# Performance work log

Measured on AMD Instinct MI355X. Metric: run time of the kernel, lower is better.

The kernel has to match this reference:

```python
import jax, jax.numpy as jnp
import numpy as np

B, IDF, CDF, H, Wd, L = 16, 128, 256, 128, 128, 64


def setup_inputs() -> dict:
    key = jax.random.key(0)
    k1, k2, k3, k4 = jax.random.split(key, 4)
    x = jax.random.normal(k1, (B, IDF, H, Wd), dtype=jnp.float32)
    context = jax.random.normal(k2, (B, CDF, L), dtype=jnp.float32)
    W = jax.random.normal(k3, (IDF, CDF), dtype=jnp.float32) * 0.02
    mask = jax.random.bernoulli(k4, 0.3, (B, L))
    # guarantee at least one unmasked word per row so the softmax is finite
    mask = mask.at[:, 0].set(False)
    return {"x": x, "context": context, "W": W, "mask": mask}


def reference(x, context, W, mask):
    # x: [B, idf, H, W]  context: [B, cdf, L]  W: [idf, cdf]  mask: [B, L] bool
    b, c, h, w = x.shape
    P = h * w
    l = context.shape[2]
    target = x.reshape(b, c, P)                       # [B, idf, P]
    # Conv1x1 over context (cdf -> idf)
    source = jnp.einsum('oc,bcl->bol', W, context)    # [B, idf, L]
    # QK^T: [B, P, idf] x [B, idf, L] -> [B, P, L]
    attn = jnp.einsum('bip,bil->bpl', target, source)
    attn = attn.reshape(b * P, l)
    # faithful to torch: mask.repeat(P, 1) tiled over the flattened rows
    m = jnp.tile(mask, (P, 1))                        # [B*P, L]
    attn = jnp.where(m, -jnp.inf, attn)
    attn = jax.nn.softmax(attn, axis=1).reshape(b, P, l)
    attnT = jnp.swapaxes(attn, 1, 2)                  # [B, L, P]
    # weighted context: [B, idf, L] x [B, L, P] -> [B, idf, P]
    weight = jnp.einsum('bil,blp->bip', source, attnT).reshape(b, c, h, w)
    attn_out = attnT.reshape(b, l, h, w)
    return weight, attn_out
```

## Files before the change

### kernel.cpp

```cpp
#include <hip/hip_runtime.h>
#include <hip/hip_bf16.h>
#include <hip/hip_fp16.h>

#define NB  16
#define IDF 128
#define CDF 256
#define LL  64
#define PP  16384
#define PXB 256
#define XPITCH 260

typedef _Float16 f16;
typedef _Float16 f16x4 __attribute__((ext_vector_type(4)));
typedef _Float16 f16x8 __attribute__((ext_vector_type(8)));
typedef float    f32x4 __attribute__((ext_vector_type(4)));

#define BAR() do { asm volatile("s_waitcnt lgkmcnt(0)" ::: "memory"); \
                   __builtin_amdgcn_s_barrier(); } while (0)

__global__ void src_pack_kernel(const float* __restrict__ Wm,
                                const float* __restrict__ ctx,
                                f16* __restrict__ srcF,
                                f16* __restrict__ srcT,
                                const unsigned char* __restrict__ mask_raw,
                                unsigned long long* __restrict__ mbits) {
    if (blockIdx.x == 0) {
        __shared__ int is_u8;
        const int tid = threadIdx.x;
        if (tid == 0) is_u8 = 0;
        if (tid < 16) mbits[tid] = 0ULL;
        __syncthreads();
        unsigned char byt[4];
        #pragma unroll
        for (int q = 0; q < 4; ++q) {
            int k = tid + q * 256;
            byt[q] = mask_raw[k];
            if ((k & 3) != 0 && byt[q] != 0) atomicOr(&is_u8, 1);
        }
        __syncthreads();
        #pragma unroll
        for (int q = 0; q < 4; ++q) {
            int k = tid + q * 256;
            int masked;
            if (is_u8) masked = (byt[q] != 0);
            else       masked = (((const int*)mask_raw)[k] != 0);
            if (masked) atomicOr(&mbits[k >> 6], 1ULL << (unsigned)(k & 63));
        }
    }

    int g = blockIdx.x * 256 + threadIdx.x;
    int l = g & (LL - 1);
    int i = (g >> 6) & (IDF - 1);
    int b = g >> 13;
    const float* wrow = Wm + (size_t)i * CDF;
    const float* ccol = ctx + (size_t)b * CDF * LL + l;
    float s = 0.f;
    #pragma unroll 8
    for (int c = 0; c < CDF; ++c)
        s = fmaf(wrow[c], ccol[(size_t)c * LL], s);
    f16 h = (f16)s;
    srcF[g] = h;
    srcT[((size_t)b * LL + l) * IDF + i] = h;
}

__global__ __launch_bounds__(256, 2)
void attn_mfma_kernel(const float* __restrict__ x,
                      const f16* __restrict__ srcT,
                      const f16* __restrict__ srcF,
                      const unsigned long long* __restrict__ mbits,
                      float* __restrict__ weight,
                      float* __restrict__ attn_out) {
    __shared__ __align__(16) unsigned char s_srcT[LL * 256];
    __shared__ __align__(16) unsigned char s_srcF[IDF * 128];
    __shared__ __align__(16) unsigned char s_u[34816];

    float* s_xpA = (float*)s_u;
    float* s_xpB = (float*)(s_u + 16640);

    const int b    = blockIdx.y;
    const int tid  = threadIdx.x;
    const int wv   = tid >> 6;
    const int lane = tid & 63;
    const int c    = lane & 15;
    const int g    = lane >> 4;
    const int cs   = (c & 7) << 4;

    f16* s_pw = (f16*)s_u + (size_t)wv * (64 * 68);

    const int bxs = (blockIdx.x & 7) * 4 + (blockIdx.x >> 3);
    const int pwb = bxs * (2 * PXB);
    const float* xb0 = x + (size_t)b * IDF * PP + pwb + wv * 64 + c;
    const float* xb1 = xb0 + PXB;

    unsigned mlo[4], mhi[4];
    #pragma unroll
    for (int r = 0; r < 4; ++r) {
        unsigned long long m = mbits[4 * g + r];
        mlo[r] = (unsigned)m;
        mhi[r] = (unsigned)(m >> 32);
    }

    float xfa[32], xfb[32];
    f16x8 xh0[4], xh1[4];
    f32x4 acc[4][4];
    f16x8 pa[4][2];

#define QK_LOAD(BUF, KS, XB)                                                \
    {   _Pragma("unroll")                                                   \
        for (int pt = 0; pt < 4; ++pt)                                      \
            _Pragma("unroll")                                               \
            for (int j = 0; j < 8; ++j)                                     \
                BUF[pt * 8 + j] =                                           \
                    (XB)[(size_t)((KS) * 32 + 8 * g + j) * PP + pt * 16];   \
    }

#define QK_CONV(BUF, XH)                                                    \
    {   _Pragma("unroll")                                                   \
        for (int pt = 0; pt < 4; ++pt)                                      \
            _Pragma("unroll")                                               \
            for (int j = 0; j < 8; ++j) XH[pt][j] = (f16)BUF[pt * 8 + j];   \
    }

#define QK_STEP_H(XH, KS)                                                   \
    {   _Pragma("unroll")                                                   \
        for (int nt = 0; nt < 4; ++nt) {                                    \
            const f16x8 bt = *reinterpret_cast<const f16x8*>(               \
                s_srcT + (nt * 16 + c) * 256 + (((KS) * 64 + 16 * g) ^ cs));\
            _Pragma("unroll")                                               \
            for (int pt = 0; pt < 4; ++pt)                                  \
                acc[pt][nt] = __builtin_amdgcn_mfma_f32_16x16x32_f16(       \
                    XH[pt], bt, acc[pt][nt], 0, 0, 0);                      \
        } }

#define QK_STEP(BUF, KS)                                                    \
    {   f16x8 xa_[4];                                                       \
        QK_CONV(BUF, xa_)                                                   \
        QK_STEP_H(xa_, KS) }

#define ACC_ZERO()                                                          \
    {   _Pragma("unroll")                                                   \
        for (int pt = 0; pt < 4; ++pt)                                      \
            _Pragma("unroll")                                               \
            for (int nt = 0; nt < 4; ++nt)                                  \
                acc[pt][nt] = (f32x4){0.f, 0.f, 0.f, 0.f}; }

#define SOFTMAX()                                                           \
    {   _Pragma("unroll")                                                   \
        for (int r = 0; r < 4; ++r) {                                       \
            const unsigned m0 = (mlo[r] >> c) & 1u;                         \
            const unsigned m1 = (mlo[r] >> (16 + c)) & 1u;                  \
            const unsigned m2 = (mhi[r] >> c) & 1u;                         \
            const unsigned m3 = (mhi[r] >> (16 + c)) & 1u;                  \
            _Pragma("unroll")                                               \
            for (int pt = 0; pt < 4; ++pt) {                                \
                if (m0) acc[pt][0][r] = -INFINITY;                          \
                if (m1) acc[pt][1][r] = -INFINITY;                          \
                if (m2) acc[pt][2][r] = -INFINITY;                          \
                if (m3) acc[pt][3][r] = -INFINITY;                          \
            }                                                               \
        }                                                                   \
        _Pragma("unroll")                                                   \
        for (int pt = 0; pt < 4; ++pt) {                                    \
            _Pragma("unroll")                                               \
            for (int r = 0; r < 4; ++r) {                                   \
                float mx = fmaxf(fmaxf(acc[pt][0][r], acc[pt][1][r]),       \
                                 fmaxf(acc[pt][2][r], acc[pt][3][r]));      \
                mx = fmaxf(mx, __shfl_xor(mx, 1, 64));                      \
                mx = fmaxf(mx, __shfl_xor(mx, 2, 64));                      \
                mx = fmaxf(mx, __shfl_xor(mx, 4, 64));                      \
                mx = fmaxf(mx, __shfl_xor(mx, 8, 64));                      \
                float sum = 0.f;                                            \
                _Pragma("unroll")                                           \
                for (int nt = 0; nt < 4; ++nt) {                            \
                    float e = exp2f((acc[pt][nt][r] - mx) * 1.44269504f);   \
                    acc[pt][nt][r] = e;                                     \
                    sum += e;                                               \
                }                                                           \
                sum += __shfl_xor(sum, 1, 64);                              \
                sum += __shfl_xor(sum, 2, 64);                              \
                sum += __shfl_xor(sum, 4, 64);                              \
                sum += __shfl_xor(sum, 8, 64);                              \
                const float inv = 1.f / sum;                                \
                _Pragma("unroll")                                           \
                for (int nt = 0; nt < 4; ++nt) acc[pt][nt][r] *= inv;       \
            }                                                               \
        } }

#define PROB_EXCHANGE()                                                     \
    {   _Pragma("unroll")                                                   \
        for (int pt = 0; pt < 4; ++pt)                                      \
            _Pragma("unroll")                                               \
            for (int nt = 0; nt < 4; ++nt)                                  \
                _Pragma("unroll")                                           \
                for (int r = 0; r < 4; ++r)                                 \
                    s_pw[(pt * 16 + 4 * g + r) * 68 + nt * 16 + c] =        \
                        (f16)acc[pt][nt][r];                                \
        _Pragma("unroll")                                                   \
        for (int pt = 0; pt < 4; ++pt)                                      \
            _Pragma("unroll")                                               \
            for (int ks = 0; ks < 2; ++ks) {                                \
                const f16* pp = s_pw + (pt * 16 + c) * 68 + ks * 32 + 8 * g;\
                f16x4 lo = *reinterpret_cast<const f16x4*>(pp);             \
                f16x4 hi = *reinterpret_cast<const f16x4*>(pp + 4);         \
                f16x8 v;                                                    \
                _Pragma("unroll")                                           \
                for (int j = 0; j < 4; ++j) { v[j] = lo[j]; v[4+j] = hi[j]; } \
                pa[pt][ks] = v;                                             \
            } }

#define FILL_ATTN(NT, XP)                                                   \
    {   _Pragma("unroll")                                                   \
        for (int pt = 0; pt < 4; ++pt)                                      \
            *reinterpret_cast<f32x4*>(                                      \
                (XP) + c * XPITCH + wv * 64 + pt * 16 + 4 * g) = acc[pt][NT]; }

#define FILL_PV(CH, XP)                                                     \
    {   f32x4 a2[4];                                                        \
        _Pragma("unroll")                                                   \
        for (int pt = 0; pt < 4; ++pt) a2[pt] = (f32x4){0.f, 0.f, 0.f, 0.f};\
        _Pragma("unroll")                                                   \
        for (int ks = 0; ks < 2; ++ks) {                                    \
            const f16x8 sf = *reinterpret_cast<const f16x8*>(               \
                s_srcF + ((CH) * 16 + c) * 128 + ((ks * 64 + 16 * g) ^ cs));\
            _Pragma("unroll")                                               \
            for (int pt = 0; pt < 4; ++pt)                                  \
                a2[pt] = __builtin_amdgcn_mfma_f32_16x16x32_f16(            \
                    pa[pt][ks], sf, a2[pt], 0, 0, 0);                       \
        }                                                                   \
        _Pragma("unroll")                                                   \
        for (int pt = 0; pt < 4; ++pt)                                      \
            *reinterpret_cast<f32x4*>(                                      \
                (XP) + c * XPITCH + wv * 64 + pt * 16 + 4 * g) = a2[pt]; }

#define FILL_CHUNK(K, XP)                                                   \
    {   if ((K) < 4) { FILL_ATTN((K), (XP)) }                               \
        else         { FILL_PV((K) - 4, (XP)) } }

#define STORE_CHUNK(K, XP, AB, WB)                                          \
    {   float* dst = ((K) < 4)                                              \
            ? ((AB) + (size_t)((K) * 16) * PP)                              \
            : ((WB) + (size_t)(((K) - 4) * 16) * PP);                       \
        _Pragma("unroll")                                                   \
        for (int k2 = 0; k2 < 4; ++k2) {                                    \
            int f = tid + k2 * 256;                                         \
            int row = f >> 6, u = f & 63;                                   \
            f32x4 v = *reinterpret_cast<const f32x4*>(                      \
                (XP) + row * XPITCH + u * 4);                               \
            __builtin_nontemporal_store(v,                                  \
                reinterpret_cast<f32x4*>(dst + (size_t)row * PP + u * 4));  \
        } }

#define PIPE_STEP(K, CUR, NXT, AB, WB)                                      \
    STORE_CHUNK(K, CUR, AB, WB) FILL_CHUNK((K) + 1, NXT) BAR();

    QK_LOAD(xfa, 0, xb0)

    {
        const f16* sT = srcT + (size_t)b * LL * IDF;
        const f16* sF = srcF + (size_t)b * IDF * LL;
        #pragma unroll
        for (int it = 0; it < 4; ++it) {
            int e = (it * 256 + tid) * 8;
            int l = e >> 7, i = e & 127;
            f16x8 v = *reinterpret_cast<const f16x8*>(sT + l * IDF + i);
            *reinterpret_cast<f16x8*>(
                s_srcT + l * 256 + ((i * 2) ^ ((l & 7) << 4))) = v;
        }
        #pragma unroll
        for (int it = 0; it < 4; ++it) {
            int e = (it * 256 + tid) * 8;
            int i = e >> 6, l = e & 63;
            f16x8 v = *reinterpret_cast<const f16x8*>(sF + i * LL + l);
            *reinterpret_cast<f16x8*>(
                s_srcF + i * 128 + ((l * 2) ^ ((i & 7) << 4))) = v;
        }
    }
    BAR();

    ACC_ZERO()
    QK_LOAD(xfb, 1, xb0)
    QK_STEP(xfa, 0)
    QK_LOAD(xfa, 2, xb0)
    QK_STEP(xfb, 1)
    QK_LOAD(xfb, 3, xb0)
    QK_STEP(xfa, 2)
    QK_STEP(xfb, 3)
    SOFTMAX()
    PROB_EXCHANGE()
    BAR();

    float* abase0 = attn_out + (size_t)b * LL * PP + pwb;
    float* wbase0 = weight + (size_t)b * IDF * PP + pwb;
    float* abase1 = abase0 + PXB;
    float* wbase1 = wbase0 + PXB;

    FILL_CHUNK(0, s_xpA)
    BAR();
    PIPE_STEP(0, s_xpA, s_xpB, abase0, wbase0)
    PIPE_STEP(1, s_xpB, s_xpA, abase0, wbase0)
    PIPE_STEP(2, s_xpA, s_xpB, abase0, wbase0)
    QK_LOAD(xfa, 0, xb1)
    QK_LOAD(xfb, 1, xb1)
    PIPE_STEP(3, s_xpB, s_xpA, abase0, wbase0)
    PIPE_STEP(4, s_xpA, s_xpB, abase0, wbase0)
    PIPE_STEP(5, s_xpB, s_xpA, abase0, wbase0)
    PIPE_STEP(6, s_xpA, s_xpB, abase0, wbase0)
    QK_CONV(xfa, xh0)
    QK_CONV(xfb, xh1)
    QK_LOAD(xfa, 2, xb1)
    QK_LOAD(xfb, 3, xb1)
    PIPE_STEP(7, s_xpB, s_xpA, abase0, wbase0)
    PIPE_STEP(8, s_xpA, s_xpB, abase0, wbase0)
    PIPE_STEP(9, s_xpB, s_xpA, abase0, wbase0)
    PIPE_STEP(10, s_xpA, s_xpB, abase0, wbase0)
    STORE_CHUNK(11, s_xpB, abase0, wbase0)
    BAR();

    ACC_ZERO()
    QK_STEP_H(xh0, 0)
    QK_STEP_H(xh1, 1)
    QK_STEP(xfa, 2)
    QK_STEP(xfb, 3)
    SOFTMAX()
    PROB_EXCHANGE()
    BAR();

    FILL_CHUNK(0, s_xpA)
    BAR();
    PIPE_STEP(0, s_xpA, s_xpB, abase1, wbase1)
    PIPE_STEP(1, s_xpB, s_xpA, abase1, wbase1)
    PIPE_STEP(2, s_xpA, s_xpB, abase1, wbase1)
    PIPE_STEP(3, s_xpB, s_xpA, abase1, wbase1)
    PIPE_STEP(4, s_xpA, s_xpB, abase1, wbase1)
    PIPE_STEP(5, s_xpB, s_xpA, abase1, wbase1)
    PIPE_STEP(6, s_xpA, s_xpB, abase1, wbase1)
    PIPE_STEP(7, s_xpB, s_xpA, abase1, wbase1)
    PIPE_STEP(8, s_xpA, s_xpB, abase1, wbase1)
    PIPE_STEP(9, s_xpB, s_xpA, abase1, wbase1)
    PIPE_STEP(10, s_xpA, s_xpB, abase1, wbase1)
    STORE_CHUNK(11, s_xpB, abase1, wbase1)
}

extern "C" void kernel_launch(void* const* d_in, const int* in_sizes, int n_in,
                              void* d_out, int out_size, void* d_ws, size_t ws_size,
                              hipStream_t stream) {
    const float*         x        = (const float*)d_in[0];
    const float*         ctx      = (const float*)d_in[1];
    const float*         Wm       = (const float*)d_in[2];
    const unsigned char* mask_raw = (const unsigned char*)d_in[3];

    float* weight   = (float*)d_out;
    float* attn_out = weight + (size_t)NB * IDF * PP;

    unsigned long long* mbits = (unsigned long long*)d_ws;
    f16* srcF = (f16*)((char*)d_ws + 4096);
    f16* srcT = srcF + (size_t)NB * IDF * LL;

    src_pack_kernel<<<(NB * IDF * LL) / 256, 256, 0, stream>>>(
        Wm, ctx, srcF, srcT, mask_raw, mbits);

    dim3 grid(PP / (2 * PXB), NB);
    attn_mfma_kernel<<<grid, 256, 0, stream>>>(x, srcT, srcF, mbits, weight, attn_out);
}
```

Baseline: 77.78 us.

## Defer PV for both pixel halves into one pass with 512-wide rows

Attention probabilities for both 256-pixel halves are now kept in registers (pa0, pa1). The weight (PV) output is then computed once across 512 contiguous pixels per channel chunk and staged through a single wider LDS buffer. The aim is longer contiguous global stores and fewer sri loads/barrier phases per chunk. In exchange it holds more registers and uses single-buffered PV staging with two barriers per chunk, so store and MFMA no longer overlap, and the earlier x-prefetch conversion overlap is removed.

```diff
diff --git a/kernel.cpp b/kernel.cpp
--- a/kernel.cpp
+++ b/kernel.cpp
@@ -8,7 +8,8 @@
 #define LL  64
 #define PP  16384
 #define PXB 256
-#define XPITCH 260
+#define XPA 260
+#define XPP 516
 
 typedef _Float16 f16;
 typedef _Float16 f16x4 __attribute__((ext_vector_type(4)));
@@ -76,6 +77,7 @@
 
     float* s_xpA = (float*)s_u;
     float* s_xpB = (float*)(s_u + 16640);
+    float* s_xpP = (float*)s_u;
 
     const int b    = blockIdx.y;
     const int tid  = threadIdx.x;
@@ -101,9 +103,8 @@
     }
 
     float xfa[32], xfb[32];
-    f16x8 xh0[4], xh1[4];
     f32x4 acc[4][4];
-    f16x8 pa[4][2];
+    f16x8 pa0[4][2], pa1[4][2];
 
 #define QK_LOAD(BUF, KS, XB)                                                \
     {   _Pragma("unroll")                                                   \
@@ -114,28 +115,21 @@
                     (XB)[(size_t)((KS) * 32 + 8 * g + j) * PP + pt * 16];   \
     }
 
-#define QK_CONV(BUF, XH)                                                    \
-    {   _Pragma("unroll")                                                   \
-        for (int pt = 0; pt < 4; ++pt)                                      \
-            _Pragma("unroll")                                               \
-            for (int j = 0; j < 8; ++j) XH[pt][j] = (f16)BUF[pt * 8 + j];   \
-    }
-
-#define QK_STEP_H(XH, KS)                                                   \
-    {   _Pragma("unroll")                                                   \
+#define QK_STEP(BUF, KS)                                                    \
+    {   f16x8 xa_[4];                                                       \
+        _Pragma("unroll")                                                   \
+        for (int pt = 0; pt < 4; ++pt)                                      \
+            _Pragma("unroll")                                               \
+            for (int j = 0; j < 8; ++j) xa_[pt][j] = (f16)BUF[pt * 8 + j];  \
+        _Pragma("unroll")                                                   \
         for (int nt = 0; nt < 4; ++nt) {                                    \
             const f16x8 bt = *reinterpret_cast<const f16x8*>(               \
                 s_srcT + (nt * 16 + c) * 256 + (((KS) * 64 + 16 * g) ^ cs));\
             _Pragma("unroll")                                               \
             for (int pt = 0; pt < 4; ++pt)                                  \
                 acc[pt][nt] = __builtin_amdgcn_mfma_f32_16x16x32_f16(       \
-                    XH[pt], bt, acc[pt][nt], 0, 0, 0);                      \
+                    xa_[pt], bt, acc[pt][nt], 0, 0, 0);                     \
         } }
-
-#define QK_STEP(BUF, KS)                                                    \
-    {   f16x8 xa_[4];                                                       \
-        QK_CONV(BUF, xa_)                                                   \
-        QK_STEP_H(xa_, KS) }
 
 #define ACC_ZERO()                                                          \
     {   _Pragma("unroll")                                                   \
@@ -186,7 +180,7 @@
             }                                                               \
         } }
 
-#define PROB_EXCHANGE()                                                     \
+#define PROB_EXCHANGE(PA)                                                   \
     {   _Pragma("unroll")                                                   \
         for (int pt = 0; pt < 4; ++pt)                                      \
             _Pragma("unroll")                                               \
@@ -205,53 +199,60 @@
                 f16x8 v;                                                    \
                 _Pragma("unroll")                                           \
                 for (int j = 0; j < 4; ++j) { v[j] = lo[j]; v[4+j] = hi[j]; } \
-                pa[pt][ks] = v;                                             \
+                PA[pt][ks] = v;                                             \
             } }
 
 #define FILL_ATTN(NT, XP)                                                   \
     {   _Pragma("unroll")                                                   \
         for (int pt = 0; pt < 4; ++pt)                                      \
             *reinterpret_cast<f32x4*>(                                      \
-                (XP) + c * XPITCH + wv * 64 + pt * 16 + 4 * g) = acc[pt][NT]; }
-
-#define FILL_PV(CH, XP)                                                     \
-    {   f32x4 a2[4];                                                        \
-        _Pragma("unroll")                                                   \
-        for (int pt = 0; pt < 4; ++pt) a2[pt] = (f32x4){0.f, 0.f, 0.f, 0.f};\
-        _Pragma("unroll")                                                   \
-        for (int ks = 0; ks < 2; ++ks) {                                    \
-            const f16x8 sf = *reinterpret_cast<const f16x8*>(               \
-                s_srcF + ((CH) * 16 + c) * 128 + ((ks * 64 + 16 * g) ^ cs));\
-            _Pragma("unroll")                                               \
-            for (int pt = 0; pt < 4; ++pt)                                  \
-                a2[pt] = __builtin_amdgcn_mfma_f32_16x16x32_f16(            \
-                    pa[pt][ks], sf, a2[pt], 0, 0, 0);                       \
-        }                                                                   \
-        _Pragma("unroll")                                                   \
-        for (int pt = 0; pt < 4; ++pt)                                      \
-            *reinterpret_cast<f32x4*>(                                      \
-                (XP) + c * XPITCH + wv * 64 + pt * 16 + 4 * g) = a2[pt]; }
-
-#define FILL_CHUNK(K, XP)                                                   \
-    {   if ((K) < 4) { FILL_ATTN((K), (XP)) }                               \
-        else         { FILL_PV((K) - 4, (XP)) } }
-
-#define STORE_CHUNK(K, XP, AB, WB)                                          \
-    {   float* dst = ((K) < 4)                                              \
-            ? ((AB) + (size_t)((K) * 16) * PP)                              \
-            : ((WB) + (size_t)(((K) - 4) * 16) * PP);                       \
-        _Pragma("unroll")                                                   \
+                (XP) + c * XPA + wv * 64 + pt * 16 + 4 * g) = acc[pt][NT]; }
+
+#define STORE_A(K, XP, AB)                                                  \
+    {   _Pragma("unroll")                                                   \
         for (int k2 = 0; k2 < 4; ++k2) {                                    \
             int f = tid + k2 * 256;                                         \
             int row = f >> 6, u = f & 63;                                   \
             f32x4 v = *reinterpret_cast<const f32x4*>(                      \
-                (XP) + row * XPITCH + u * 4);                               \
+                (XP) + row * XPA + u * 4);                                  \
             __builtin_nontemporal_store(v,                                  \
-                reinterpret_cast<f32x4*>(dst + (size_t)row * PP + u * 4));  \
+                reinterpret_cast<f32x4*>((AB) + (size_t)((K) * 16 + row) * PP + u * 4)); \
         } }
 
-#define PIPE_STEP(K, CUR, NXT, AB, WB)                                      \
-    STORE_CHUNK(K, CUR, AB, WB) FILL_CHUNK((K) + 1, NXT) BAR();
+#define FILL_PV(CH)                                                         \
+    {   f32x4 a2[8];                                                        \
+        _Pragma("unroll")                                                   \
+        for (int q = 0; q < 8; ++q) a2[q] = (f32x4){0.f, 0.f, 0.f, 0.f};    \
+        _Pragma("unroll")                                                   \
+        for (int ks = 0; ks < 2; ++ks) {                                    \
+            const f16x8 sf = *reinterpret_cast<const f16x8*>(               \
+                s_srcF + ((CH) * 16 + c) * 128 + ((ks * 64 + 16 * g) ^ cs));\
+            _Pragma("unroll")                                               \
+            for (int pt = 0; pt < 4; ++pt) {                                \
+                a2[pt]     = __builtin_amdgcn_mfma_f32_16x16x32_f16(        \
+                    pa0[pt][ks], sf, a2[pt], 0, 0, 0);                      \
+                a2[4 + pt] = __builtin_amdgcn_mfma_f32_16x16x32_f16(        \
+                    pa1[pt][ks], sf, a2[4 + pt], 0, 0, 0);                  \
+            }                                                               \
+        }                                                                   \
+        _Pragma("unroll")                                                   \
+        for (int tl = 0; tl < 2; ++tl)                                      \
+            _Pragma("unroll")                                               \
+            for (int pt = 0; pt < 4; ++pt)                                  \
+                *reinterpret_cast<f32x4*>(                                  \
+                    s_xpP + c * XPP + tl * 256 + wv * 64 + pt * 16 + 4 * g) \
+                    = a2[tl * 4 + pt]; }
+
+#define STORE_PV(CH, WB)                                                    \
+    {   _Pragma("unroll")                                                   \
+        for (int k2 = 0; k2 < 8; ++k2) {                                    \
+            int f = tid + k2 * 256;                                         \
+            int row = f >> 7, u = f & 127;                                  \
+            f32x4 v = *reinterpret_cast<const f32x4*>(                      \
+                s_xpP + row * XPP + u * 4);                                 \
+            __builtin_nontemporal_store(v,                                  \
+                reinterpret_cast<f32x4*>((WB) + (size_t)((CH) * 16 + row) * PP + u * 4)); \
+        } }
 
     QK_LOAD(xfa, 0, xb0)
 
@@ -277,6 +278,10 @@
     }
     BAR();
 
+    float* abase0 = attn_out + (size_t)b * LL * PP + pwb;
+    float* abase1 = abase0 + PXB;
+    float* wbase  = weight + (size_t)b * IDF * PP + pwb;
+
     ACC_ZERO()
     QK_LOAD(xfb, 1, xb0)
     QK_STEP(xfa, 0)
@@ -286,59 +291,44 @@
     QK_STEP(xfa, 2)
     QK_STEP(xfb, 3)
     SOFTMAX()
-    PROB_EXCHANGE()
-    BAR();
-
-    float* abase0 = attn_out + (size_t)b * LL * PP + pwb;
-    float* wbase0 = weight + (size_t)b * IDF * PP + pwb;
-    float* abase1 = abase0 + PXB;
-    float* wbase1 = wbase0 + PXB;
-
-    FILL_CHUNK(0, s_xpA)
-    BAR();
-    PIPE_STEP(0, s_xpA, s_xpB, abase0, wbase0)
-    PIPE_STEP(1, s_xpB, s_xpA, abase0, wbase0)
-    PIPE_STEP(2, s_xpA, s_xpB, abase0, wbase0)
-    QK_LOAD(xfa, 0, xb1)
-    QK_LOAD(xfb, 1, xb1)
-    PIPE_STEP(3, s_xpB, s_xpA, abase0, wbase0)
-    PIPE_STEP(4, s_xpA, s_xpB, abase0, wbase0)
-    PIPE_STEP(5, s_xpB, s_xpA, abase0, wbase0)
-    PIPE_STEP(6, s_xpA, s_xpB, abase0, wbase0)
-    QK_CONV(xfa, xh0)
-    QK_CONV(xfb, xh1)
+    PROB_EXCHANGE(pa0)
+    BAR();
+
+    FILL_ATTN(0, s_xpA)
+    BAR();
+    STORE_A(0, s_xpA, abase0) QK_LOAD(xfa, 0, xb1) FILL_ATTN(1, s_xpB) BAR();
+    STORE_A(1, s_xpB, abase0) QK_LOAD(xfb, 1, xb1) FILL_ATTN(2, s_xpA) BAR();
+    STORE_A(2, s_xpA, abase0) FILL_ATTN(3, s_xpB) BAR();
+    STORE_A(3, s_xpB, abase0)
+    BAR();
+
+    ACC_ZERO()
+    QK_STEP(xfa, 0)
     QK_LOAD(xfa, 2, xb1)
+    QK_STEP(xfb, 1)
     QK_LOAD(xfb, 3, xb1)
-    PIPE_STEP(7, s_xpB, s_xpA, abase0, wbase0)
-    PIPE_STEP(8, s_xpA, s_xpB, abase0, wbase0)
-    PIPE_STEP(9, s_xpB, s_xpA, abase0, wbase0)
-    PIPE_STEP(10, s_xpA, s_xpB, abase0, wbase0)
-    STORE_CHUNK(11, s_xpB, abase0, wbase0)
-    BAR();
-
-    ACC_ZERO()
-    QK_STEP_H(xh0, 0)
-    QK_STEP_H(xh1, 1)
     QK_STEP(xfa, 2)
     QK_STEP(xfb, 3)
     SOFTMAX()
-    PROB_EXCHANGE()
-    BAR();
-
-    FILL_CHUNK(0, s_xpA)
-    BAR();
-    PIPE_STEP(0, s_xpA, s_xpB, abase1, wbase1)
-    PIPE_STEP(1, s_xpB, s_xpA, abase1, wbase1)
-    PIPE_STEP(2, s_xpA, s_xpB, abase1, wbase1)
-    PIPE_STEP(3, s_xpB, s_xpA, abase1, wbase1)
-    PIPE_STEP(4, s_xpA, s_xpB, abase1, wbase1)
-    PIPE_STEP(5, s_xpB, s_xpA, abase1, wbase1)
-    PIPE_STEP(6, s_xpA, s_xpB, abase1, wbase1)
-    PIPE_STEP(7, s_xpB, s_xpA, abase1, wbase1)
-    PIPE_STEP(8, s_xpA, s_xpB, abase1, wbase1)
-    PIPE_STEP(9, s_xpB, s_xpA, abase1, wbase1)
-    PIPE_STEP(10, s_xpA, s_xpB, abase1, wbase1)
-    STORE_CHUNK(11, s_xpB, abase1, wbase1)
+    PROB_EXCHANGE(pa1)
+    BAR();
+
+    FILL_ATTN(0, s_xpA)
+    BAR();
+    STORE_A(0, s_xpA, abase1) FILL_ATTN(1, s_xpB) BAR();
+    STORE_A(1, s_xpB, abase1) FILL_ATTN(2, s_xpA) BAR();
+    STORE_A(2, s_xpA, abase1) FILL_ATTN(3, s_xpB) BAR();
+    STORE_A(3, s_xpB, abase1)
+    BAR();
+
+    FILL_PV(0) BAR(); STORE_PV(0, wbase) BAR();
+    FILL_PV(1) BAR(); STORE_PV(1, wbase) BAR();
+    FILL_PV(2) BAR(); STORE_PV(2, wbase) BAR();
+    FILL_PV(3) BAR(); STORE_PV(3, wbase) BAR();
+    FILL_PV(4) BAR(); STORE_PV(4, wbase) BAR();
+    FILL_PV(5) BAR(); STORE_PV(5, wbase) BAR();
+    FILL_PV(6) BAR(); STORE_PV(6, wbase) BAR();
+    FILL_PV(7) BAR(); STORE_PV(7, wbase)
 }
 
 extern "C" void kernel_launch(void* const* d_in, const int* in_sizes, int n_in,
```

After: 81.63 us. +5.0%, slower.
